# Optimization experiments

Measured on AMD Instinct MI355X. Metric: run time of the kernel, lower is better.

## Reference

```python
import jax, jax.numpy as jnp
import numpy as np

NUM_HEADS = 8
EPS = 1e-6


def setup_inputs() -> dict:
    key = jax.random.key(0)
    k1, k2, k3 = jax.random.split(key, 3)
    B, N, C = 4, 256, 512
    x = jax.random.normal(k1, (B, N, C), dtype=jnp.float32)
    w_qkv = jax.random.normal(k2, (3 * C, C), dtype=jnp.float32) * (C ** -0.5)
    w_proj = jax.random.normal(k3, (C, C), dtype=jnp.float32) * (C ** -0.5)
    b_proj = jnp.zeros((C,), dtype=jnp.float32)
    paramR = jnp.ones((1,), dtype=jnp.float32)
    return {"x": x, "w_qkv": w_qkv, "w_proj": w_proj, "b_proj": b_proj, "paramR": paramR}


def _fourier_attention(x, w_qkv, w_proj, b_proj, paramR):
    B, N, C = x.shape
    H = NUM_HEADS
    Dh = C // H
    # qkv projection (no bias), split into per-head q,k,v: (B,H,N,Dh)
    qkv = jnp.einsum('bnc,kc->bnk', x, w_qkv).reshape(B, N, 3, H, Dh)
    q = qkv[:, :, 0].transpose(0, 2, 1, 3)
    k = qkv[:, :, 1].transpose(0, 2, 1, 3)
    v = qkv[:, :, 2].transpose(0, 2, 1, 3)
    R = paramR[0]
    # Generalized Fourier integral kernel: prod_d sin(R*(q_d - k_d))/(q_d - k_d)
    diff = q[:, :, :, None, :] - k[:, :, None, :, :]  # (B,H,Nq,Nk,Dh)
    near0 = jnp.abs(diff) < 1e-8
    safe = jnp.where(near0, jnp.float32(1.0), diff)
    s = jnp.where(near0, R, jnp.sin(R * safe) / safe)
    score = jnp.prod(s, axis=-1)  # (B,H,Nq,Nk)
    a4 = score ** 4
    attn = a4 / (jnp.sum(a4, axis=-1, keepdims=True) + EPS)  # normalize over keys
    out = jnp.einsum('bhqk,bhkd->bhqd', attn, v)
    out = out.transpose(0, 2, 1, 3).reshape(B, N, C)
    return jnp.einsum('bnc,oc->bno', out, w_proj) + b_proj


def reference(x, w_qkv, w_proj, b_proj, paramR):
    return _fourier_attention(x, w_qkv, w_proj, b_proj, paramR)
```

## Files before the change

kernel.cpp:

```cpp
#include <hip/hip_runtime.h>
#include <math.h>

#define BB 4
#define NN 256
#define CC 512
#define HH 8
#define DH 64

typedef __attribute__((ext_vector_type(8))) short bf16x8;
typedef __attribute__((ext_vector_type(4))) float f32x4;
typedef __attribute__((ext_vector_type(2))) float f32x2;

__device__ inline unsigned short f2bf(float f) {
  unsigned u = __float_as_uint(f);
  u += 0x7FFFu + ((u >> 16) & 1u);
  return (unsigned short)(u >> 16);
}
__device__ inline float bf2f(unsigned short s) {
  return __uint_as_float((unsigned)s << 16);
}

__global__ __launch_bounds__(256) void cvt_hilo3(
    const float* __restrict__ in0, unsigned short* __restrict__ h0,
    unsigned short* __restrict__ l0, const float* __restrict__ in1,
    unsigned short* __restrict__ h1, unsigned short* __restrict__ l1,
    const float* __restrict__ in2, unsigned short* __restrict__ h2,
    unsigned short* __restrict__ l2) {
  int b = blockIdx.x;
  const float* in;
  unsigned short *h, *l;
  if (b < 512) {
    in = in0; h = h0; l = l0;
  } else if (b < 1280) {
    in = in1; h = h1; l = l1; b -= 512;
  } else {
    in = in2; h = h2; l = l2; b -= 1280;
  }
  int i = (b * 256 + threadIdx.x) * 4;
  float4 f = *(const float4*)(in + i);
  float fa[4] = {f.x, f.y, f.z, f.w};
  ushort4 hv, lv;
  unsigned short* hp = (unsigned short*)&hv;
  unsigned short* lp = (unsigned short*)&lv;
#pragma unroll
  for (int j = 0; j < 4; j++) {
    unsigned short hb = f2bf(fa[j]);
    hp[j] = hb;
    lp[j] = f2bf(fa[j] - bf2f(hb));
  }
  *(ushort4*)(h + i) = hv;
  *(ushort4*)(l + i) = lv;
}

template <bool BIAS>
__global__ __launch_bounds__(256, 2) void gemm_mfma(
    const unsigned short* __restrict__ Ah, const unsigned short* __restrict__ Al,
    const unsigned short* __restrict__ Bh, const unsigned short* __restrict__ Bl,
    const float* __restrict__ bias, float* __restrict__ C, int M, int N,
    int K) {
  __shared__ unsigned short sAh[2][64][72], sAl[2][64][72];
  __shared__ unsigned short sBh[2][64][72], sBl[2][64][72];
  const int t = threadIdx.x;
  const int lane = t & 63;
  const int w = t >> 6;
  const int bm = blockIdx.y * 64;
  const int bn = blockIdx.x * 64;
  const int wr = (w >> 1) * 32;
  const int wc = (w & 1) * 32;
  const int quad = lane >> 4;
  const int l16 = lane & 15;

  const int r0 = t >> 3;
  const int r1 = r0 + 32;
  const int c8 = (t & 7) * 8;

  const size_t a0 = (size_t)(bm + r0) * K + c8;
  const size_t a1 = (size_t)(bm + r1) * K + c8;
  const size_t b0 = (size_t)(bn + r0) * K + c8;
  const size_t b1 = (size_t)(bn + r1) * K + c8;

  f32x4 acc[2][2];
#pragma unroll
  for (int i = 0; i < 2; i++)
#pragma unroll
    for (int j = 0; j < 2; j++) {
      acc[i][j][0] = 0.f;
      acc[i][j][1] = 0.f;
      acc[i][j][2] = 0.f;
      acc[i][j][3] = 0.f;
    }

  uint4 pa0, pa1, pa2, pa3, pb0, pb1, pb2, pb3;
#define GLOADS(K0)                       \
  pa0 = *(const uint4*)(Ah + a0 + (K0)); \
  pa1 = *(const uint4*)(Ah + a1 + (K0)); \
  pa2 = *(const uint4*)(Al + a0 + (K0)); \
  pa3 = *(const uint4*)(Al + a1 + (K0)); \
  pb0 = *(const uint4*)(Bh + b0 + (K0)); \
  pb1 = *(const uint4*)(Bh + b1 + (K0)); \
  pb2 = *(const uint4*)(Bl + b0 + (K0)); \
  pb3 = *(const uint4*)(Bl + b1 + (K0));

#define STORE(P)                  \
  *(uint4*)&sAh[P][r0][c8] = pa0; \
  *(uint4*)&sAh[P][r1][c8] = pa1; \
  *(uint4*)&sAl[P][r0][c8] = pa2; \
  *(uint4*)&sAl[P][r1][c8] = pa3; \
  *(uint4*)&sBh[P][r0][c8] = pb0; \
  *(uint4*)&sBh[P][r1][c8] = pb1; \
  *(uint4*)&sBl[P][r0][c8] = pb2; \
  *(uint4*)&sBl[P][r1][c8] = pb3;

  GLOADS(0)
  STORE(0)
  __syncthreads();
  GLOADS(64)

  int p = 0;
  for (int k0 = 0; k0 < K; k0 += 64) {
#pragma unroll
    for (int kk = 0; kk < 2; kk++) {
      const int kc = kk * 32 + quad * 8;
      bf16x8 ah[2], al[2], bh[2], bl[2];
#pragma unroll
      for (int i = 0; i < 2; i++) {
        ah[i] = *(const bf16x8*)&sAh[p][wr + i * 16 + l16][kc];
        al[i] = *(const bf16x8*)&sAl[p][wr + i * 16 + l16][kc];
        bh[i] = *(const bf16x8*)&sBh[p][wc + i * 16 + l16][kc];
        bl[i] = *(const bf16x8*)&sBl[p][wc + i * 16 + l16][kc];
      }
#pragma unroll
      for (int i = 0; i < 2; i++)
#pragma unroll
        for (int j = 0; j < 2; j++) {
          acc[i][j] = __builtin_amdgcn_mfma_f32_16x16x32_bf16(
              ah[i], bh[j], acc[i][j], 0, 0, 0);
          acc[i][j] = __builtin_amdgcn_mfma_f32_16x16x32_bf16(
              ah[i], bl[j], acc[i][j], 0, 0, 0);
          acc[i][j] = __builtin_amdgcn_mfma_f32_16x16x32_bf16(
              al[i], bh[j], acc[i][j], 0, 0, 0);
        }
    }
    if (k0 + 64 < K) {
      STORE(p ^ 1)
      if (k0 + 128 < K) {
        GLOADS(k0 + 128)
      }
    }
    __syncthreads();
    p ^= 1;
  }
#undef GLOADS
#undef STORE

#pragma unroll
  for (int i = 0; i < 2; i++)
#pragma unroll
    for (int j = 0; j < 2; j++) {
      int n = bn + wc + j * 16 + l16;
      float bv = BIAS ? bias[n] : 0.f;
#pragma unroll
      for (int r = 0; r < 4; r++) {
        int m = bm + wr + i * 16 + quad * 4 + r;
        C[(size_t)m * N + n] = acc[i][j][r] + bv;
      }
    }
}

__global__ __launch_bounds__(512, 4) void fourier_attn(
    const float* __restrict__ qkv, const float* __restrict__ paramR,
    unsigned short* __restrict__ aoh, unsigned short* __restrict__ aol) {
  __shared__ float Kt[64][68];
  __shared__ float Vs[64][68];
  __shared__ float Qs[16][64];
  __shared__ unsigned short Pah[16][72];
  __shared__ unsigned short Pal[16][72];
  __shared__ float Sden[16];
  __shared__ f32x4 Red[4][64];

  const int t = threadIdx.x;
  const int lane = t & 63;
  const int wv = t >> 6;
  const int quad = lane >> 4;
  const int l16 = lane & 15;
  const int qc = blockIdx.x;
  const int h = blockIdx.y;
  const int b = blockIdx.z;
  const float R = paramR[0];
  const float cR = R * 0.15915494309189535f;

  const float* base = qkv + (size_t)b * NN * (3 * CC) + h * DH;

  if (t < 256) {
    int r = t >> 4;
    int c4 = (t & 15) << 2;
    *(float4*)&Qs[r][c4] =
        *(const float4*)(base + (size_t)(qc * 16 + r) * (3 * CC) + c4);
  }

  const int qi0 = wv * 2, qi1 = wv * 2 + 1;
  float Sp[2] = {0.f, 0.f};
  f32x4 oacc;
  oacc[0] = 0.f; oacc[1] = 0.f; oacc[2] = 0.f; oacc[3] = 0.f;

  const int nc = wv & 3;
  const int g2 = wv >> 2;
  const int kb = g2 * 32 + quad * 8;

  float4 pk[2], pv[2];
#define LOADT(JT)                                                   \
  _Pragma("unroll") for (int u0 = 0; u0 < 2; u0++) {                \
    int u = t + 512 * u0;                                           \
    int r_ = u >> 4;                                                \
    int c4_ = (u & 15) << 2;                                        \
    const float* row_ = base + (size_t)((JT) * 64 + r_) * (3 * CC); \
    pk[u0] = *(const float4*)(row_ + CC + c4_);                     \
    pv[u0] = *(const float4*)(row_ + 2 * CC + c4_);                 \
  }

  LOADT(0)

  const f32x2 eps2 = {1e-30f, 1e-30f};
  const f32x2 cR2 = {cR, cR};

  for (int jt = 0; jt < 4; jt++) {
    __syncthreads();
#pragma unroll
    for (int u0 = 0; u0 < 2; u0++) {
      int u = t + 512 * u0;
      int r = u >> 4;
      int c4 = (u & 15) << 2;
      *(float4*)&Kt[r][c4] = pk[u0];
      *(float4*)&Vs[r][c4] = pv[u0];
    }
    __syncthreads();
    if (jt < 3) {
      LOADT(jt + 1)
    }

    f32x2 nmA0 = {1.f, 1.f}, nmB0 = {1.f, 1.f};
    f32x2 nmA1 = {1.f, 1.f}, nmB1 = {1.f, 1.f};
    f32x2 dnA0 = {1.f, 1.f}, dnB0 = {1.f, 1.f};
    f32x2 dnA1 = {1.f, 1.f}, dnB1 = {1.f, 1.f};
#pragma unroll
    for (int d4 = 0; d4 < 16; d4++) {
      float4 k4 = *(const float4*)&Kt[lane][4 * d4];
      float4 qa = *(const float4*)&Qs[qi0][4 * d4];
      float4 qb = *(const float4*)&Qs[qi1][4 * d4];
      f32x2 kA = {k4.x, k4.y};
      f32x2 kB = {k4.z, k4.w};
      f32x2 dA0 = ((f32x2){qa.x, qa.y} - kA) + eps2;
      f32x2 dB0 = ((f32x2){qa.z, qa.w} - kB) + eps2;
      f32x2 dA1 = ((f32x2){qb.x, qb.y} - kA) + eps2;
      f32x2 dB1 = ((f32x2){qb.z, qb.w} - kB) + eps2;
      f32x2 gA0 = cR2 * dA0, gB0 = cR2 * dB0;
      f32x2 gA1 = cR2 * dA1, gB1 = cR2 * dB1;
      f32x2 sA0, sB0, sA1, sB1;
      sA0.x = __builtin_amdgcn_sinf(gA0.x);
      sA0.y = __builtin_amdgcn_sinf(gA0.y);
      sB0.x = __builtin_amdgcn_sinf(gB0.x);
      sB0.y = __builtin_amdgcn_sinf(gB0.y);
      sA1.x = __builtin_amdgcn_sinf(gA1.x);
      sA1.y = __builtin_amdgcn_sinf(gA1.y);
      sB1.x = __builtin_amdgcn_sinf(gB1.x);
      sB1.y = __builtin_amdgcn_sinf(gB1.y);
      nmA0 *= sA0;
      nmB0 *= sB0;
      nmA1 *= sA1;
      nmB1 *= sB1;
      dnA0 *= dA0;
      dnB0 *= dB0;
      dnA1 *= dA1;
      dnB1 *= dB1;
    }
    {
      f32x2 n0 = nmA0 * nmB0, d0 = dnA0 * dnB0;
      f32x2 n1 = nmA1 * nmB1, d1 = dnA1 * dnB1;
      float sc0 = (n0.x * n0.y) / (d0.x * d0.y);
      float sc1 = (n1.x * n1.y) / (d1.x * d1.y);
      float t0 = sc0 * sc0, t1 = sc1 * sc1;
      float a40 = t0 * t0, a41 = t1 * t1;
      Sp[0] += a40;
      Sp[1] += a41;
      unsigned short h0 = f2bf(a40), h1 = f2bf(a41);
      Pah[qi0][lane] = h0;
      Pal[qi0][lane] = f2bf(a40 - bf2f(h0));
      Pah[qi1][lane] = h1;
      Pal[qi1][lane] = f2bf(a41 - bf2f(h1));
    }
    __syncthreads();

    {
      bf16x8 pah = *(const bf16x8*)&Pah[l16][kb];
      bf16x8 pal = *(const bf16x8*)&Pal[l16][kb];
      bf16x8 vh, vl;
#pragma unroll
      for (int j = 0; j < 8; j++) {
        float f = Vs[kb + j][nc * 16 + l16];
        unsigned short hb = f2bf(f);
        vh[j] = (short)hb;
        vl[j] = (short)f2bf(f - bf2f(hb));
      }
      oacc = __builtin_amdgcn_mfma_f32_16x16x32_bf16(pah, vh, oacc, 0, 0, 0);
      oacc = __builtin_amdgcn_mfma_f32_16x16x32_bf16(pah, vl, oacc, 0, 0, 0);
      oacc = __builtin_amdgcn_mfma_f32_16x16x32_bf16(pal, vh, oacc, 0, 0, 0);
    }
  }
#undef LOADT

#pragma unroll
  for (int q = 0; q < 2; q++) {
    float s = Sp[q];
#pragma unroll
    for (int off = 32; off > 0; off >>= 1) s += __shfl_xor(s, off, 64);
    if (lane == 0) Sden[qi0 + q] = s;
  }
  if (wv >= 4) Red[wv - 4][lane] = oacc;
  __syncthreads();
  if (wv < 4) {
    f32x4 part = Red[wv][lane];
#pragma unroll
    for (int r = 0; r < 4; r++) {
      int q = quad * 4 + r;
      float s = Sden[q];
      float o = (oacc[r] + part[r]) / (s + 1e-6f);
      int n = qc * 16 + q;
      size_t idx = (size_t)(b * NN + n) * CC + h * DH + nc * 16 + l16;
      unsigned short oh = f2bf(o);
      aoh[idx] = oh;
      aol[idx] = f2bf(o - bf2f(oh));
    }
  }
}

extern "C" void kernel_launch(void* const* d_in, const int* in_sizes, int n_in,
                              void* d_out, int out_size, void* d_ws,
                              size_t ws_size, hipStream_t stream) {
  const float* x = (const float*)d_in[0];
  const float* w_qkv = (const float*)d_in[1];
  const float* w_proj = (const float*)d_in[2];
  const float* b_proj = (const float*)d_in[3];
  const float* paramR = (const float*)d_in[4];
  float* outp = (float*)d_out;

  const int nX = BB * NN * CC;
  const int nWq = 3 * CC * CC;
  const int nWp = CC * CC;

  unsigned short* xh = (unsigned short*)d_ws;
  unsigned short* xl = xh + nX;
  unsigned short* wqh = xl + nX;
  unsigned short* wql = wqh + nWq;
  unsigned short* wph = wql + nWq;
  unsigned short* wpl = wph + nWp;
  unsigned short* aoh = wpl + nWp;
  unsigned short* aol = aoh + nX;
  float* qkv_ws = (float*)(aol + nX);

  cvt_hilo3<<<1536, 256, 0, stream>>>(x, xh, xl, w_qkv, wqh, wql, w_proj, wph,
                                      wpl);

  gemm_mfma<false><<<dim3(3 * CC / 64, BB * NN / 64), 256, 0, stream>>>(
      xh, xl, wqh, wql, nullptr, qkv_ws, BB * NN, 3 * CC, CC);

  fourier_attn<<<dim3(NN / 16, HH, BB), 512, 0, stream>>>(qkv_ws, paramR, aoh,
                                                          aol);

  gemm_mfma<true><<<dim3(CC / 64, BB * NN / 64), 256, 0, stream>>>(
      aoh, aol, wph, wpl, b_proj, outp, BB * NN, CC, CC);
}
```

Before: 123.3 us.

## Fuse bf16 hi/lo conversion into GEMMs and split attention over key halves

Drops the separate hi/lo bf16 conversion kernel, so the GEMMs now load fp32 inputs and split them into hi/lo bf16 while staging into shared memory. The attention kernel is split across two key-range halves, doubling the grid, and writes unnormalized numerators and denominators. The projection GEMM then sums the two partials and normalizes while loading its A tile. This removes one launch and the bf16 workspace round-trip and raises attention parallelism, at the cost of extra fp32 partial traffic and conversion work repeated per GEMM tile. It also raises the attention occupancy hint and sets MFMA priority.

New measurement: 130.9 us. 1.06x slower.

```diff
diff --git a/kernel.cpp b/kernel.cpp
--- a/kernel.cpp
+++ b/kernel.cpp
@@ -1,4 +1,5 @@
 #include <hip/hip_runtime.h>
+#include <hip/hip_bf16.h>
 #include <math.h>
 
 #define BB 4
@@ -20,44 +21,36 @@
   return __uint_as_float((unsigned)s << 16);
 }
 
-__global__ __launch_bounds__(256) void cvt_hilo3(
-    const float* __restrict__ in0, unsigned short* __restrict__ h0,
-    unsigned short* __restrict__ l0, const float* __restrict__ in1,
-    unsigned short* __restrict__ h1, unsigned short* __restrict__ l1,
-    const float* __restrict__ in2, unsigned short* __restrict__ h2,
-    unsigned short* __restrict__ l2) {
-  int b = blockIdx.x;
-  const float* in;
-  unsigned short *h, *l;
-  if (b < 512) {
-    in = in0; h = h0; l = l0;
-  } else if (b < 1280) {
-    in = in1; h = h1; l = l1; b -= 512;
-  } else {
-    in = in2; h = h2; l = l2; b -= 1280;
-  }
-  int i = (b * 256 + threadIdx.x) * 4;
-  float4 f = *(const float4*)(in + i);
-  float fa[4] = {f.x, f.y, f.z, f.w};
-  ushort4 hv, lv;
-  unsigned short* hp = (unsigned short*)&hv;
-  unsigned short* lp = (unsigned short*)&lv;
-#pragma unroll
-  for (int j = 0; j < 4; j++) {
-    unsigned short hb = f2bf(fa[j]);
-    hp[j] = hb;
-    lp[j] = f2bf(fa[j] - bf2f(hb));
-  }
-  *(ushort4*)(h + i) = hv;
-  *(ushort4*)(l + i) = lv;
-}
-
-template <bool BIAS>
-__global__ __launch_bounds__(256, 2) void gemm_mfma(
-    const unsigned short* __restrict__ Ah, const unsigned short* __restrict__ Al,
-    const unsigned short* __restrict__ Bh, const unsigned short* __restrict__ Bl,
-    const float* __restrict__ bias, float* __restrict__ C, int M, int N,
-    int K) {
+__device__ inline float4 f4add(float4 a, float4 b) {
+  return make_float4(a.x + b.x, a.y + b.y, a.z + b.z, a.w + b.w);
+}
+__device__ inline float4 f4scale(float4 a, float s) {
+  return make_float4(a.x * s, a.y * s, a.z * s, a.w * s);
+}
+
+__device__ inline void hilo2(float a, float b, unsigned& hu, unsigned& lu) {
+  __hip_bfloat162 h2 = __float22bfloat162_rn(make_float2(a, b));
+  float2 hf = __bfloat1622float2(h2);
+  __hip_bfloat162 l2 = __float22bfloat162_rn(make_float2(a - hf.x, b - hf.y));
+  __builtin_memcpy(&hu, &h2, 4);
+  __builtin_memcpy(&lu, &l2, 4);
+}
+__device__ inline void cvt8(float4 f0, float4 f1, uint4& hv, uint4& lv) {
+  unsigned h0, h1, h2, h3, l0, l1, l2, l3;
+  hilo2(f0.x, f0.y, h0, l0);
+  hilo2(f0.z, f0.w, h1, l1);
+  hilo2(f1.x, f1.y, h2, l2);
+  hilo2(f1.z, f1.w, h3, l3);
+  hv = make_uint4(h0, h1, h2, h3);
+  lv = make_uint4(l0, l1, l2, l3);
+}
+
+template <bool COMBINE, bool BIAS>
+__global__ __launch_bounds__(256, 2) void gemm_f32(
+    const float* __restrict__ A0, const float* __restrict__ A1,
+    const float* __restrict__ dn0, const float* __restrict__ dn1,
+    const float* __restrict__ Bw, const float* __restrict__ bias,
+    float* __restrict__ C, int M, int N, int K) {
   __shared__ unsigned short sAh[2][64][72], sAl[2][64][72];
   __shared__ unsigned short sBh[2][64][72], sBl[2][64][72];
   const int t = threadIdx.x;
@@ -90,29 +83,60 @@
       acc[i][j][3] = 0.f;
     }
 
-  uint4 pa0, pa1, pa2, pa3, pb0, pb1, pb2, pb3;
-#define GLOADS(K0)                       \
-  pa0 = *(const uint4*)(Ah + a0 + (K0)); \
-  pa1 = *(const uint4*)(Ah + a1 + (K0)); \
-  pa2 = *(const uint4*)(Al + a0 + (K0)); \
-  pa3 = *(const uint4*)(Al + a1 + (K0)); \
-  pb0 = *(const uint4*)(Bh + b0 + (K0)); \
-  pb1 = *(const uint4*)(Bh + b1 + (K0)); \
-  pb2 = *(const uint4*)(Bl + b0 + (K0)); \
-  pb3 = *(const uint4*)(Bl + b1 + (K0));
-
-#define STORE(P)                  \
-  *(uint4*)&sAh[P][r0][c8] = pa0; \
-  *(uint4*)&sAh[P][r1][c8] = pa1; \
-  *(uint4*)&sAl[P][r0][c8] = pa2; \
-  *(uint4*)&sAl[P][r1][c8] = pa3; \
-  *(uint4*)&sBh[P][r0][c8] = pb0; \
-  *(uint4*)&sBh[P][r1][c8] = pb1; \
-  *(uint4*)&sBl[P][r0][c8] = pb2; \
-  *(uint4*)&sBl[P][r1][c8] = pb3;
+  float4 pa0, pa1, pa2, pa3, pb0, pb1, pb2, pb3;
+  float4 qa0, qa1, qa2, qa3;
+  float pd0 = 0.f, pd1 = 0.f;
+
+#define GLOADS(K0)                                      \
+  pa0 = *(const float4*)(A0 + a0 + (K0));               \
+  pa1 = *(const float4*)(A0 + a0 + (K0) + 4);           \
+  pa2 = *(const float4*)(A0 + a1 + (K0));               \
+  pa3 = *(const float4*)(A0 + a1 + (K0) + 4);           \
+  pb0 = *(const float4*)(Bw + b0 + (K0));               \
+  pb1 = *(const float4*)(Bw + b0 + (K0) + 4);           \
+  pb2 = *(const float4*)(Bw + b1 + (K0));               \
+  pb3 = *(const float4*)(Bw + b1 + (K0) + 4);           \
+  if (COMBINE) {                                        \
+    qa0 = *(const float4*)(A1 + a0 + (K0));             \
+    qa1 = *(const float4*)(A1 + a0 + (K0) + 4);         \
+    qa2 = *(const float4*)(A1 + a1 + (K0));             \
+    qa3 = *(const float4*)(A1 + a1 + (K0) + 4);         \
+    const int hd_ = (K0) >> 6;                          \
+    pd0 = dn0[(size_t)(bm + r0) * HH + hd_] +           \
+          dn1[(size_t)(bm + r0) * HH + hd_];            \
+    pd1 = dn0[(size_t)(bm + r1) * HH + hd_] +           \
+          dn1[(size_t)(bm + r1) * HH + hd_];            \
+  }
+
+#define STOREP(P)                              \
+  {                                            \
+    float4 fa0 = pa0, fa1 = pa1;               \
+    float4 fa2 = pa2, fa3 = pa3;               \
+    if (COMBINE) {                             \
+      float i0 = 1.f / (pd0 + 1e-6f);          \
+      float i1 = 1.f / (pd1 + 1e-6f);          \
+      fa0 = f4scale(f4add(fa0, qa0), i0);      \
+      fa1 = f4scale(f4add(fa1, qa1), i0);      \
+      fa2 = f4scale(f4add(fa2, qa2), i1);      \
+      fa3 = f4scale(f4add(fa3, qa3), i1);      \
+    }                                          \
+    uint4 hv, lv;                              \
+    cvt8(fa0, fa1, hv, lv);                    \
+    *(uint4*)&sAh[P][r0][c8] = hv;             \
+    *(uint4*)&sAl[P][r0][c8] = lv;             \
+    cvt8(fa2, fa3, hv, lv);                    \
+    *(uint4*)&sAh[P][r1][c8] = hv;             \
+    *(uint4*)&sAl[P][r1][c8] = lv;             \
+    cvt8(pb0, pb1, hv, lv);                    \
+    *(uint4*)&sBh[P][r0][c8] = hv;             \
+    *(uint4*)&sBl[P][r0][c8] = lv;             \
+    cvt8(pb2, pb3, hv, lv);                    \
+    *(uint4*)&sBh[P][r1][c8] = hv;             \
+    *(uint4*)&sBl[P][r1][c8] = lv;             \
+  }
 
   GLOADS(0)
-  STORE(0)
+  STOREP(0)
   __syncthreads();
   GLOADS(64)
 
@@ -142,7 +166,7 @@
         }
     }
     if (k0 + 64 < K) {
-      STORE(p ^ 1)
+      STOREP(p ^ 1)
       if (k0 + 128 < K) {
         GLOADS(k0 + 128)
       }
@@ -151,7 +175,7 @@
     p ^= 1;
   }
 #undef GLOADS
-#undef STORE
+#undef STOREP
 
 #pragma unroll
   for (int i = 0; i < 2; i++)
@@ -167,15 +191,15 @@
     }
 }
 
-__global__ __launch_bounds__(512, 4) void fourier_attn(
+__global__ __launch_bounds__(512, 6) void fourier_attn(
     const float* __restrict__ qkv, const float* __restrict__ paramR,
-    unsigned short* __restrict__ aoh, unsigned short* __restrict__ aol) {
+    float* __restrict__ num0, float* __restrict__ num1,
+    float* __restrict__ den0, float* __restrict__ den1) {
   __shared__ float Kt[64][68];
   __shared__ float Vs[64][68];
   __shared__ float Qs[16][64];
   __shared__ unsigned short Pah[16][72];
   __shared__ unsigned short Pal[16][72];
-  __shared__ float Sden[16];
   __shared__ f32x4 Red[4][64];
 
   const int t = threadIdx.x;
@@ -183,9 +207,10 @@
   const int wv = t >> 6;
   const int quad = lane >> 4;
   const int l16 = lane & 15;
-  const int qc = blockIdx.x;
-  const int h = blockIdx.y;
-  const int b = blockIdx.z;
+  const int h = blockIdx.x & 7;
+  const int b = blockIdx.x >> 3;
+  const int qc = blockIdx.y >> 1;
+  const int kc = blockIdx.y & 1;
   const float R = paramR[0];
   const float cR = R * 0.15915494309189535f;
 
@@ -218,12 +243,12 @@
     pv[u0] = *(const float4*)(row_ + 2 * CC + c4_);                 \
   }
 
-  LOADT(0)
+  LOADT(kc * 2)
 
   const f32x2 eps2 = {1e-30f, 1e-30f};
   const f32x2 cR2 = {cR, cR};
 
-  for (int jt = 0; jt < 4; jt++) {
+  for (int jj = 0; jj < 2; jj++) {
     __syncthreads();
 #pragma unroll
     for (int u0 = 0; u0 < 2; u0++) {
@@ -234,8 +259,8 @@
       *(float4*)&Vs[r][c4] = pv[u0];
     }
     __syncthreads();
-    if (jt < 3) {
-      LOADT(jt + 1)
+    if (jj == 0) {
+      LOADT(kc * 2 + 1)
     }
 
     f32x2 nmA0 = {1.f, 1.f}, nmB0 = {1.f, 1.f};
@@ -301,19 +326,26 @@
         vh[j] = (short)hb;
         vl[j] = (short)f2bf(f - bf2f(hb));
       }
+      __builtin_amdgcn_s_setprio(1);
       oacc = __builtin_amdgcn_mfma_f32_16x16x32_bf16(pah, vh, oacc, 0, 0, 0);
       oacc = __builtin_amdgcn_mfma_f32_16x16x32_bf16(pah, vl, oacc, 0, 0, 0);
       oacc = __builtin_amdgcn_mfma_f32_16x16x32_bf16(pal, vh, oacc, 0, 0, 0);
+      __builtin_amdgcn_s_setprio(0);
     }
   }
 #undef LOADT
 
+  float* nump = kc ? num1 : num0;
+  float* denp = kc ? den1 : den0;
 #pragma unroll
   for (int q = 0; q < 2; q++) {
     float s = Sp[q];
 #pragma unroll
     for (int off = 32; off > 0; off >>= 1) s += __shfl_xor(s, off, 64);
-    if (lane == 0) Sden[qi0 + q] = s;
+    if (lane == 0) {
+      int m = b * NN + qc * 16 + qi0 + q;
+      denp[(size_t)m * HH + h] = s;
+    }
   }
   if (wv >= 4) Red[wv - 4][lane] = oacc;
   __syncthreads();
@@ -322,13 +354,8 @@
 #pragma unroll
     for (int r = 0; r < 4; r++) {
       int q = quad * 4 + r;
-      float s = Sden[q];
-      float o = (oacc[r] + part[r]) / (s + 1e-6f);
-      int n = qc * 16 + q;
-      size_t idx = (size_t)(b * NN + n) * CC + h * DH + nc * 16 + l16;
-      unsigned short oh = f2bf(o);
-      aoh[idx] = oh;
-      aol[idx] = f2bf(o - bf2f(oh));
+      int m = b * NN + qc * 16 + q;
+      nump[(size_t)m * CC + h * DH + nc * 16 + l16] = oacc[r] + part[r];
     }
   }
 }
@@ -344,28 +371,20 @@
   float* outp = (float*)d_out;
 
   const int nX = BB * NN * CC;
-  const int nWq = 3 * CC * CC;
-  const int nWp = CC * CC;
-
-  unsigned short* xh = (unsigned short*)d_ws;
-  unsigned short* xl = xh + nX;
-  unsigned short* wqh = xl + nX;
-  unsigned short* wql = wqh + nWq;
-  unsigned short* wph = wql + nWq;
-  unsigned short* wpl = wph + nWp;
-  unsigned short* aoh = wpl + nWp;
-  unsigned short* aol = aoh + nX;
-  float* qkv_ws = (float*)(aol + nX);
-
-  cvt_hilo3<<<1536, 256, 0, stream>>>(x, xh, xl, w_qkv, wqh, wql, w_proj, wph,
-                                      wpl);
-
-  gemm_mfma<false><<<dim3(3 * CC / 64, BB * NN / 64), 256, 0, stream>>>(
-      xh, xl, wqh, wql, nullptr, qkv_ws, BB * NN, 3 * CC, CC);
-
-  fourier_attn<<<dim3(NN / 16, HH, BB), 512, 0, stream>>>(qkv_ws, paramR, aoh,
-                                                          aol);
-
-  gemm_mfma<true><<<dim3(CC / 64, BB * NN / 64), 256, 0, stream>>>(
-      aoh, aol, wph, wpl, b_proj, outp, BB * NN, CC, CC);
-}
+
+  float* qkv_ws = (float*)d_ws;
+  float* num0 = qkv_ws + 1024 * 1536;
+  float* num1 = num0 + nX;
+  float* den0 = num1 + nX;
+  float* den1 = den0 + 1024 * HH;
+
+  gemm_f32<false, false><<<dim3(3 * CC / 64, BB * NN / 64), 256, 0, stream>>>(
+      x, nullptr, nullptr, nullptr, w_qkv, nullptr, qkv_ws, BB * NN, 3 * CC,
+      CC);
+
+  fourier_attn<<<dim3(HH * BB, (NN / 16) * 2), 512, 0, stream>>>(
+      qkv_ws, paramR, num0, num1, den0, den1);
+
+  gemm_f32<true, true><<<dim3(CC / 64, BB * NN / 64), 256, 0, stream>>>(
+      num0, num1, den0, den1, w_proj, b_proj, outp, BB * NN, CC, CC);
+}
```

## Split attention keys across two blocks and combine with a normalization kernel

Applied to the files above, without the earlier changes.

The attention kernel now splits the 256 keys into two halves handled by separate blocks, doubling the grid from 512 to 1024 blocks. Each block writes unnormalized partial numerators and denominators, and a new combine_norm kernel sums them, divides, and produces the hi/lo bf16 split. V is loaded straight from global memory into registers instead of being staged in LDS, launch bounds ask for 8 blocks per CU, and MFMA issue priority is raised. The aim is more parallelism and occupancy for a compute-bound sin-heavy kernel, at the cost of an extra launch and extra global traffic for the partials.

Result: slower. 293.5 us (+138.0%).

```diff
diff --git a/kernel.cpp b/kernel.cpp
--- a/kernel.cpp
+++ b/kernel.cpp
@@ -167,15 +167,14 @@
     }
 }
 
-__global__ __launch_bounds__(512, 4) void fourier_attn(
+__global__ __launch_bounds__(512, 8) void fourier_attn(
     const float* __restrict__ qkv, const float* __restrict__ paramR,
-    unsigned short* __restrict__ aoh, unsigned short* __restrict__ aol) {
+    float* __restrict__ num0, float* __restrict__ num1,
+    float* __restrict__ den0, float* __restrict__ den1) {
   __shared__ float Kt[64][68];
-  __shared__ float Vs[64][68];
   __shared__ float Qs[16][64];
   __shared__ unsigned short Pah[16][72];
   __shared__ unsigned short Pal[16][72];
-  __shared__ float Sden[16];
   __shared__ f32x4 Red[4][64];
 
   const int t = threadIdx.x;
@@ -183,9 +182,10 @@
   const int wv = t >> 6;
   const int quad = lane >> 4;
   const int l16 = lane & 15;
-  const int qc = blockIdx.x;
-  const int h = blockIdx.y;
-  const int b = blockIdx.z;
+  const int h = blockIdx.x & 7;
+  const int b = blockIdx.x >> 3;
+  const int qc = blockIdx.y >> 1;
+  const int kc = blockIdx.y & 1;
   const float R = paramR[0];
   const float cR = R * 0.15915494309189535f;
 
@@ -206,24 +206,26 @@
   const int nc = wv & 3;
   const int g2 = wv >> 2;
   const int kb = g2 * 32 + quad * 8;
-
-  float4 pk[2], pv[2];
-#define LOADT(JT)                                                   \
-  _Pragma("unroll") for (int u0 = 0; u0 < 2; u0++) {                \
-    int u = t + 512 * u0;                                           \
-    int r_ = u >> 4;                                                \
-    int c4_ = (u & 15) << 2;                                        \
-    const float* row_ = base + (size_t)((JT) * 64 + r_) * (3 * CC); \
-    pk[u0] = *(const float4*)(row_ + CC + c4_);                     \
-    pv[u0] = *(const float4*)(row_ + 2 * CC + c4_);                 \
-  }
-
-  LOADT(0)
+  const int vcol = nc * 16 + l16;
+
+  float4 pk[2];
+#define LOADK(JT)                                                         \
+  _Pragma("unroll") for (int u0 = 0; u0 < 2; u0++) {                      \
+    int u = t + 512 * u0;                                                 \
+    int r_ = u >> 4;                                                      \
+    int c4_ = (u & 15) << 2;                                              \
+    pk[u0] =                                                              \
+        *(const float4*)(base + (size_t)((JT) * 64 + r_) * (3 * CC) + CC + \
+                         c4_);                                            \
+  }
+
+  LOADK(kc * 2)
 
   const f32x2 eps2 = {1e-30f, 1e-30f};
   const f32x2 cR2 = {cR, cR};
 
-  for (int jt = 0; jt < 4; jt++) {
+  for (int jj = 0; jj < 2; jj++) {
+    const int jt = kc * 2 + jj;
     __syncthreads();
 #pragma unroll
     for (int u0 = 0; u0 < 2; u0++) {
@@ -231,11 +233,10 @@
       int r = u >> 4;
       int c4 = (u & 15) << 2;
       *(float4*)&Kt[r][c4] = pk[u0];
-      *(float4*)&Vs[r][c4] = pv[u0];
     }
     __syncthreads();
-    if (jt < 3) {
-      LOADT(jt + 1)
+    if (jj == 0) {
+      LOADK(kc * 2 + 1)
     }
 
     f32x2 nmA0 = {1.f, 1.f}, nmB0 = {1.f, 1.f};
@@ -273,6 +274,13 @@
       dnA1 *= dA1;
       dnB1 *= dB1;
     }
+
+    float vf[8];
+#pragma unroll
+    for (int j = 0; j < 8; j++) {
+      vf[j] = base[(size_t)(jt * 64 + kb + j) * (3 * CC) + 2 * CC + vcol];
+    }
+
     {
       f32x2 n0 = nmA0 * nmB0, d0 = dnA0 * dnB0;
       f32x2 n1 = nmA1 * nmB1, d1 = dnA1 * dnB1;
@@ -296,24 +304,31 @@
       bf16x8 vh, vl;
 #pragma unroll
       for (int j = 0; j < 8; j++) {
-        float f = Vs[kb + j][nc * 16 + l16];
+        float f = vf[j];
         unsigned short hb = f2bf(f);
         vh[j] = (short)hb;
         vl[j] = (short)f2bf(f - bf2f(hb));
       }
+      __builtin_amdgcn_s_setprio(1);
       oacc = __builtin_amdgcn_mfma_f32_16x16x32_bf16(pah, vh, oacc, 0, 0, 0);
       oacc = __builtin_amdgcn_mfma_f32_16x16x32_bf16(pah, vl, oacc, 0, 0, 0);
       oacc = __builtin_amdgcn_mfma_f32_16x16x32_bf16(pal, vh, oacc, 0, 0, 0);
-    }
-  }
-#undef LOADT
-
+      __builtin_amdgcn_s_setprio(0);
+    }
+  }
+#undef LOADK
+
+  float* nump = kc ? num1 : num0;
+  float* denp = kc ? den1 : den0;
 #pragma unroll
   for (int q = 0; q < 2; q++) {
     float s = Sp[q];
 #pragma unroll
     for (int off = 32; off > 0; off >>= 1) s += __shfl_xor(s, off, 64);
-    if (lane == 0) Sden[qi0 + q] = s;
+    if (lane == 0) {
+      int m = b * NN + qc * 16 + qi0 + q;
+      denp[(size_t)m * HH + h] = s;
+    }
   }
   if (wv >= 4) Red[wv - 4][lane] = oacc;
   __syncthreads();
@@ -322,15 +337,35 @@
 #pragma unroll
     for (int r = 0; r < 4; r++) {
       int q = quad * 4 + r;
-      float s = Sden[q];
-      float o = (oacc[r] + part[r]) / (s + 1e-6f);
-      int n = qc * 16 + q;
-      size_t idx = (size_t)(b * NN + n) * CC + h * DH + nc * 16 + l16;
-      unsigned short oh = f2bf(o);
-      aoh[idx] = oh;
-      aol[idx] = f2bf(o - bf2f(oh));
-    }
-  }
+      int m = b * NN + qc * 16 + q;
+      nump[(size_t)m * CC + h * DH + nc * 16 + l16] = oacc[r] + part[r];
+    }
+  }
+}
+
+__global__ __launch_bounds__(256) void combine_norm(
+    const float* __restrict__ num0, const float* __restrict__ num1,
+    const float* __restrict__ den0, const float* __restrict__ den1,
+    unsigned short* __restrict__ aoh, unsigned short* __restrict__ aol) {
+  int e = (blockIdx.x * 256 + threadIdx.x) * 4;
+  int m = e >> 9;
+  int hd = (e >> 6) & 7;
+  float den = den0[(size_t)m * HH + hd] + den1[(size_t)m * HH + hd] + 1e-6f;
+  float4 n0 = *(const float4*)(num0 + e);
+  float4 n1 = *(const float4*)(num1 + e);
+  float o[4] = {(n0.x + n1.x) / den, (n0.y + n1.y) / den,
+                (n0.z + n1.z) / den, (n0.w + n1.w) / den};
+  ushort4 hv, lv;
+  unsigned short* hp = (unsigned short*)&hv;
+  unsigned short* lp = (unsigned short*)&lv;
+#pragma unroll
+  for (int j = 0; j < 4; j++) {
+    unsigned short hb = f2bf(o[j]);
+    hp[j] = hb;
+    lp[j] = f2bf(o[j] - bf2f(hb));
+  }
+  *(ushort4*)(aoh + e) = hv;
+  *(ushort4*)(aol + e) = lv;
 }
 
 extern "C" void kernel_launch(void* const* d_in, const int* in_sizes, int n_in,
@@ -356,6 +391,10 @@
   unsigned short* aoh = wpl + nWp;
   unsigned short* aol = aoh + nX;
   float* qkv_ws = (float*)(aol + nX);
+  float* num0 = qkv_ws + 1024 * 1536;
+  float* num1 = num0 + nX;
+  float* den0 = num1 + nX;
+  float* den1 = den0 + 1024 * HH;
 
   cvt_hilo3<<<1536, 256, 0, stream>>>(x, xh, xl, w_qkv, wqh, wql, w_proj, wph,
                                       wpl);
@@ -363,8 +402,11 @@
   gemm_mfma<false><<<dim3(3 * CC / 64, BB * NN / 64), 256, 0, stream>>>(
       xh, xl, wqh, wql, nullptr, qkv_ws, BB * NN, 3 * CC, CC);
 
-  fourier_attn<<<dim3(NN / 16, HH, BB), 512, 0, stream>>>(qkv_ws, paramR, aoh,
-                                                          aol);
+  fourier_attn<<<dim3(HH * BB, (NN / 16) * 2), 512, 0, stream>>>(
+      qkv_ws, paramR, num0, num1, den0, den1);
+
+  combine_norm<<<nX / 1024, 256, 0, stream>>>(num0, num1, den0, den1, aoh,
+                                              aol);
 
   gemm_mfma<true><<<dim3(CC / 64, BB * NN / 64), 256, 0, stream>>>(
       aoh, aol, wph, wpl, b_proj, outp, BB * NN, CC, CC);
```
